# Kernel optimization log

Hardware: AMD Instinct MI355X
Metric: run time of the kernel (lower is better)

## Reference

```python
import jax, jax.numpy as jnp
import numpy as np

H = 128  # GRU hidden dim

def gru_sequence(x_emb, W_ih, W_hh, b_ih, b_hh):
    """Run a GRU over x_emb (S, B, E); return final-step output (B, H).
    Matches torch.nn.GRU gate math:
      r = sig(W_ir x + b_ir + W_hr h + b_hr)
      z = sig(W_iz x + b_iz + W_hz h + b_hz)
      n = tanh(W_in x + b_in + r * (W_hn h + b_hn))
      h' = (1 - z) * n + z * h
    """
    S, B, E = x_emb.shape
    # Precompute input projections for all timesteps: (S, B, 3H)
    gx_all = jnp.einsum('sbe,ge->sbg', x_emb, W_ih) + b_ih

    def step(h, gx):
        gh = h @ W_hh.T + b_hh               # (B, 3H)
        r = jax.nn.sigmoid(gx[:, :H] + gh[:, :H])
        z = jax.nn.sigmoid(gx[:, H:2*H] + gh[:, H:2*H])
        n = jnp.tanh(gx[:, 2*H:] + r * gh[:, 2*H:])
        h_new = (1.0 - z) * n + z * h
        return h_new, None

    h0 = jnp.zeros((B, H), dtype=x_emb.dtype)
    h_final, _ = jax.lax.scan(step, h0, gx_all)
    return h_final  # (B, H) == out at last timestep


def setup_inputs() -> dict:
    key = jax.random.key(0)
    ks = jax.random.split(key, 12)
    S, B, V, E = 512, 512, 50000, 50
    x1 = jax.random.randint(ks[0], (S, B), 0, V, dtype=jnp.int32)
    x2 = jax.random.randint(ks[1], (S, B), 0, V, dtype=jnp.int32)
    emb = jax.random.uniform(ks[2], (V, E), jnp.float32, -0.01, 0.01)
    s = 1.0 / np.sqrt(H)
    W_ih = jax.random.uniform(ks[3], (3*H, E), jnp.float32, -s, s)
    W_hh = jax.random.uniform(ks[4], (3*H, H), jnp.float32, -s, s)
    b_ih = jax.random.uniform(ks[5], (3*H,), jnp.float32, -s, s)
    b_hh = jax.random.uniform(ks[6], (3*H,), jnp.float32, -s, s)
    s1 = 1.0 / np.sqrt(2*H)
    W1 = jax.random.uniform(ks[7], (H, 2*H), jnp.float32, -s1, s1)
    b1 = jax.random.uniform(ks[8], (H,), jnp.float32, -s1, s1)
    s2 = 1.0 / np.sqrt(H)
    W2 = jax.random.uniform(ks[9], (1, H), jnp.float32, -s2, s2)
    b2 = jax.random.uniform(ks[10], (1,), jnp.float32, -s2, s2)
    return {"x1": x1, "x2": x2, "emb": emb, "W_ih": W_ih, "W_hh": W_hh,
            "b_ih": b_ih, "b_hh": b_hh, "W1": W1, "b1": b1, "W2": W2, "b2": b2}


def reference(x1, x2, emb, W_ih, W_hh, b_ih, b_hh, W1, b1, W2, b2):
    e1 = emb[x1]  # (S, B, E)
    e2 = emb[x2]
    h1 = gru_sequence(e1, W_ih, W_hh, b_ih, b_hh)  # (B, H)
    h2 = gru_sequence(e2, W_ih, W_hh, b_ih, b_hh)  # (B, H)
    fc_in = jnp.concatenate([h1, h2], axis=-1)     # (B, 2H)
    hid = jax.nn.relu(fc_in @ W1.T + b1)
    out = jax.nn.sigmoid(hid @ W2.T + b2)          # (B, 1)
    return out
```

## Files before the change

### kernel.cpp

```cpp
#include <hip/hip_runtime.h>
#include <hip/hip_bf16.h>
#include <stdint.h>

#define S_LEN 512
#define BATCH 512
#define HID   128
#define G3    384
#define EMB   50
#define VOC   50000

typedef __attribute__((ext_vector_type(8))) short short8;
typedef __attribute__((ext_vector_type(4))) float float4v;

__device__ inline unsigned short f2bf(float f) {
  union { float f; uint32_t u; } v; v.f = f;
  uint32_t u = v.u;
  u += 0x7fffu + ((u >> 16) & 1u);
  return (unsigned short)(u >> 16);
}
__device__ inline float bf2f(unsigned short h) {
  union { uint32_t u; float f; } v; v.u = ((uint32_t)h) << 16;
  return v.f;
}
__device__ inline uint32_t fbits(float f) {
  union { float f; uint32_t u; } v; v.f = f; return v.u;
}
__device__ inline float fast_sig(float x) {
  return __builtin_amdgcn_rcpf(1.f + __expf(-x));
}

__device__ inline short8 load8_bf_padded(const float* __restrict__ row, int k0) {
  float f[8];
  if (k0 + 7 < EMB) {
    float4v a = *(const float4v*)(row + k0);
    float4v b = *(const float4v*)(row + k0 + 4);
#pragma unroll
    for (int i = 0; i < 4; ++i) { f[i] = a[i]; f[i + 4] = b[i]; }
  } else {
#pragma unroll
    for (int i = 0; i < 8; ++i) f[i] = (k0 + i < EMB) ? row[k0 + i] : 0.f;
  }
  short8 s;
#pragma unroll
  for (int i = 0; i < 8; ++i) s[i] = (short)f2bf(f[i]);
  return s;
}

__global__ __launch_bounds__(256) void build_gxv(
    const float* __restrict__ emb, const float* __restrict__ W_ih,
    const float* __restrict__ b_ih, const float* __restrict__ b_hh,
    unsigned short* __restrict__ gxv) {
  __shared__ __align__(16) unsigned short cmat[64][392];
  const int w  = threadIdx.x >> 6;
  const int L  = threadIdx.x & 63;
  const int q  = L >> 4;
  const int ln = L & 15;
  const int vbase = blockIdx.x * 64 + w * 16;
  const int vloc  = w * 16;

  const int vr = min(vbase + ln, VOC - 1);
  const float* arow = emb + (size_t)vr * EMB;
  short8 afr0 = load8_bf_padded(arow, q * 8);
  short8 afr1 = load8_bf_padded(arow, 32 + q * 8);

  for (int nt = 0; nt < 24; ++nt) {
    const int gg = nt * 16 + ln;
    const float* brow = W_ih + (size_t)gg * EMB;
    short8 b0 = load8_bf_padded(brow, q * 8);
    short8 b1 = load8_bf_padded(brow, 32 + q * 8);
    const float bias = b_ih[gg] + (gg < 256 ? b_hh[gg] : 0.f);
    float4v acc = {bias, bias, bias, bias};
    acc = __builtin_amdgcn_mfma_f32_16x16x32_bf16(afr0, b0, acc, 0, 0, 0);
    acc = __builtin_amdgcn_mfma_f32_16x16x32_bf16(afr1, b1, acc, 0, 0, 0);
#pragma unroll
    for (int r = 0; r < 4; ++r)
      cmat[vloc + q * 4 + r][gg] = f2bf(acc[r]);
  }
  __syncthreads();

  for (int idx = threadIdx.x; idx < 3072; idx += 256) {
    const int row = idx / 48, c8 = idx - row * 48;
    const int vrow = blockIdx.x * 64 + row;
    if (vrow < VOC) {
      short8 v = *(const short8*)(&cmat[row][c8 * 8]);
      *(short8*)(gxv + (size_t)vrow * G3 + c8 * 8) = v;
    }
  }
}

__global__ __launch_bounds__(512) void gru_kernel(
    const int* __restrict__ x1, const int* __restrict__ x2,
    const unsigned short* __restrict__ gxv, const float* __restrict__ W_hh,
    const float* __restrict__ b_hh, float* __restrict__ fcin) {
  const int bid   = blockIdx.x;
  const int gru   = bid >> 7;
  const int chunk = bid & 127;
  const int* xs   = gru ? x2 : x1;

  const int tid = threadIdx.x;
  const int w  = tid >> 6;
  const int L  = tid & 63;
  const int q  = L >> 4;
  const int ln = L & 15;
  const int jb = w * 16;
  const int jl = L >> 2, n = L & 3;
  const int j  = jb + jl;
  const int ng = chunk * 4 + n;

  __shared__ __align__(16) unsigned short hbuf[2][512];
  __shared__ float scr[3][128][4];

  short8 afrag[3][4];
#pragma unroll
  for (int t = 0; t < 3; ++t) {
    const float* wr = W_hh + (size_t)(t * 128 + jb + ln) * HID;
#pragma unroll
    for (int kf = 0; kf < 4; ++kf) {
      const int k0 = kf * 32 + q * 8;
      float4v f0 = *(const float4v*)(wr + k0);
      float4v f1 = *(const float4v*)(wr + k0 + 4);
      short8 a;
#pragma unroll
      for (int i = 0; i < 4; ++i) a[i] = (short)f2bf(f0[i]);
#pragma unroll
      for (int i = 0; i < 4; ++i) a[i + 4] = (short)f2bf(f1[i]);
      afrag[t][kf] = a;
    }
  }

  const float bhn = b_hh[2 * 128 + j];

  for (int idx = tid; idx < 1024; idx += 512) ((unsigned short*)hbuf)[idx] = 0;

  float h = 0.f;

  const int tok0 = xs[ng];
  unsigned short gxr, gxz, gxnn;
  {
    const unsigned short* gp = gxv + (size_t)tok0 * G3;
    gxr = gp[j]; gxz = gp[128 + j]; gxnn = gp[256 + j];
  }
  int tok1 = xs[BATCH + ng];

  const int wofs = (((j >> 3) * 4 + n) << 3) + (j & 7);
  const int rofs = ((q * 4 + (ln & 3)) << 3);

  __syncthreads();

  for (int s = 0; s < S_LEN; ++s) {
    unsigned short pr, pz, pn;
    {
      const unsigned short* gp = gxv + (size_t)tok1 * G3;
      pr = gp[j]; pz = gp[128 + j]; pn = gp[256 + j];
    }
    const int s2 = (s + 2 < S_LEN) ? (s + 2) : 0;
    const int tok2 = xs[s2 * BATCH + ng];

    const unsigned short* rb = hbuf[s & 1];
    short8 bfrag[4];
#pragma unroll
    for (int kf = 0; kf < 4; ++kf)
      bfrag[kf] = *(const short8*)(rb + kf * 128 + rofs);

    float4v acc[3];
#pragma unroll
    for (int t = 0; t < 3; ++t) {
      float4v a0 = {0.f, 0.f, 0.f, 0.f};
      float4v a1 = {0.f, 0.f, 0.f, 0.f};
      a0 = __builtin_amdgcn_mfma_f32_16x16x32_bf16(afrag[t][0], bfrag[0], a0, 0, 0, 0);
      a1 = __builtin_amdgcn_mfma_f32_16x16x32_bf16(afrag[t][1], bfrag[1], a1, 0, 0, 0);
      a0 = __builtin_amdgcn_mfma_f32_16x16x32_bf16(afrag[t][2], bfrag[2], a0, 0, 0, 0);
      a1 = __builtin_amdgcn_mfma_f32_16x16x32_bf16(afrag[t][3], bfrag[3], a1, 0, 0, 0);
      acc[t] = a0 + a1;
    }

    if (ln < 4) {
#pragma unroll
      for (int t = 0; t < 3; ++t)
#pragma unroll
        for (int r = 0; r < 4; ++r)
          scr[t][jb + q * 4 + r][ln] = acc[t][r];
    }
    const float aR = scr[0][j][n];
    const float aZ = scr[1][j][n];
    const float aN = scr[2][j][n];

    const float gr  = bf2f(gxr) + aR;
    const float gz  = bf2f(gxz) + aZ;
    const float ghn = aN + bhn;
    const float rg  = fast_sig(gr);
    const float zg  = fast_sig(gz);
    const float pre = bf2f(gxnn) + rg * ghn;
    const float nn  = 2.f * fast_sig(2.f * pre) - 1.f;
    h = zg * (h - nn) + nn;

    hbuf[(s + 1) & 1][wofs] = (unsigned short)((fbits(h) + 0x8000u) >> 16);

    asm volatile("s_waitcnt lgkmcnt(0)\n\ts_barrier" ::: "memory");

    gxr = pr; gxz = pz; gxnn = pn;
    tok1 = tok2;
  }

  fcin[(size_t)ng * 256 + gru * 128 + j] = h;
}

__global__ __launch_bounds__(128) void head_kernel(
    const float* __restrict__ fcin, const float* __restrict__ W1,
    const float* __restrict__ b1, const float* __restrict__ W2,
    const float* __restrict__ b2, float* __restrict__ out) {
  __shared__ float fc[256];
  __shared__ float part[2];
  const int b = blockIdx.x, t = threadIdx.x;
  fc[t]       = fcin[(size_t)b * 256 + t];
  fc[t + 128] = fcin[(size_t)b * 256 + t + 128];
  __syncthreads();

  float acc = b1[t];
#pragma unroll 8
  for (int k = 0; k < 256; ++k) acc += W1[t * 256 + k] * fc[k];
  const float hid = fmaxf(acc, 0.f);

  float v = hid * W2[t];
#pragma unroll
  for (int o = 32; o > 0; o >>= 1) v += __shfl_xor(v, o, 64);
  if ((t & 63) == 0) part[t >> 6] = v;
  __syncthreads();
  if (t == 0) {
    const float s = part[0] + part[1] + b2[0];
    out[b] = fast_sig(s);
  }
}

extern "C" void kernel_launch(void* const* d_in, const int* in_sizes, int n_in,
                              void* d_out, int out_size, void* d_ws, size_t ws_size,
                              hipStream_t stream) {
  const int*   x1   = (const int*)d_in[0];
  const int*   x2   = (const int*)d_in[1];
  const float* emb  = (const float*)d_in[2];
  const float* W_ih = (const float*)d_in[3];
  const float* W_hh = (const float*)d_in[4];
  const float* b_ih = (const float*)d_in[5];
  const float* b_hh = (const float*)d_in[6];
  const float* W1   = (const float*)d_in[7];
  const float* b1   = (const float*)d_in[8];
  const float* W2   = (const float*)d_in[9];
  const float* b2   = (const float*)d_in[10];
  float* out = (float*)d_out;

  unsigned short* gxv = (unsigned short*)d_ws;
  float* fcin = (float*)((char*)d_ws + (size_t)VOC * G3 * 2);

  build_gxv<<<(VOC + 63) / 64, 256, 0, stream>>>(emb, W_ih, b_ih, b_hh, gxv);
  gru_kernel<<<256, 512, 0, stream>>>(x1, x2, gxv, W_hh, b_hh, fcin);
  head_kernel<<<512, 128, 0, stream>>>(fcin, W1, b1, W2, b2, out);
}
```

Measured before the change: 414.3 us.

## Fold exp2 scaling into weights, transpose gate scratch, and prefetch W_ih tiles

Pre-scales W_ih, W_hh and the biases by -log2(e) (or -2·log2(e) for the n gate), so the recurrent step can apply exp2 directly with no multiply before the sigmoid and tanh. The b_hn bias is loaded into the MFMA accumulator instead of being added afterwards. The gate scratch buffer is transposed and padded so each lane stores a float4 vector instead of four scalar stores. build_gxv also software-prefetches the next W_ih tile. The per-step dependency chain gets shorter, but bf16 rounding now applies to the scaled weights, which shifts numerics slightly.

```diff
diff --git a/kernel.cpp b/kernel.cpp
--- a/kernel.cpp
+++ b/kernel.cpp
@@ -9,6 +9,9 @@
 #define EMB   50
 #define VOC   50000
 
+#define NL2E  (-1.4426950408889634f)
+#define N2L2E (-2.8853900817779268f)
+
 typedef __attribute__((ext_vector_type(8))) short short8;
 typedef __attribute__((ext_vector_type(4))) float float4v;
 
@@ -29,7 +32,8 @@
   return __builtin_amdgcn_rcpf(1.f + __expf(-x));
 }
 
-__device__ inline short8 load8_bf_padded(const float* __restrict__ row, int k0) {
+__device__ inline short8 load8_bf_padded(const float* __restrict__ row, int k0,
+                                         float sc) {
   float f[8];
   if (k0 + 7 < EMB) {
     float4v a = *(const float4v*)(row + k0);
@@ -42,7 +46,7 @@
   }
   short8 s;
 #pragma unroll
-  for (int i = 0; i < 8; ++i) s[i] = (short)f2bf(f[i]);
+  for (int i = 0; i < 8; ++i) s[i] = (short)f2bf(f[i] * sc);
   return s;
 }
 
@@ -60,21 +64,32 @@
 
   const int vr = min(vbase + ln, VOC - 1);
   const float* arow = emb + (size_t)vr * EMB;
-  short8 afr0 = load8_bf_padded(arow, q * 8);
-  short8 afr1 = load8_bf_padded(arow, 32 + q * 8);
+  short8 afr0 = load8_bf_padded(arow, q * 8, 1.f);
+  short8 afr1 = load8_bf_padded(arow, 32 + q * 8, 1.f);
+
+  int gg = ln;
+  float sc = NL2E;
+  short8 b0 = load8_bf_padded(W_ih + (size_t)gg * EMB, q * 8, sc);
+  short8 b1 = load8_bf_padded(W_ih + (size_t)gg * EMB, 32 + q * 8, sc);
+  float bias = sc * (b_ih[gg] + b_hh[gg]);
 
   for (int nt = 0; nt < 24; ++nt) {
-    const int gg = nt * 16 + ln;
-    const float* brow = W_ih + (size_t)gg * EMB;
-    short8 b0 = load8_bf_padded(brow, q * 8);
-    short8 b1 = load8_bf_padded(brow, 32 + q * 8);
-    const float bias = b_ih[gg] + (gg < 256 ? b_hh[gg] : 0.f);
+    short8 nb0, nb1; float nbias;
+    if (nt < 23) {
+      const int g2 = (nt + 1) * 16 + ln;
+      const float s2 = (g2 < 256) ? NL2E : N2L2E;
+      const float* brow = W_ih + (size_t)g2 * EMB;
+      nb0 = load8_bf_padded(brow, q * 8, s2);
+      nb1 = load8_bf_padded(brow, 32 + q * 8, s2);
+      nbias = s2 * (b_ih[g2] + (g2 < 256 ? b_hh[g2] : 0.f));
+    }
     float4v acc = {bias, bias, bias, bias};
     acc = __builtin_amdgcn_mfma_f32_16x16x32_bf16(afr0, b0, acc, 0, 0, 0);
     acc = __builtin_amdgcn_mfma_f32_16x16x32_bf16(afr1, b1, acc, 0, 0, 0);
 #pragma unroll
     for (int r = 0; r < 4; ++r)
       cmat[vloc + q * 4 + r][gg] = f2bf(acc[r]);
+    gg += 16; b0 = nb0; b1 = nb1; bias = nbias;
   }
   __syncthreads();
 
@@ -108,11 +123,12 @@
   const int ng = chunk * 4 + n;
 
   __shared__ __align__(16) unsigned short hbuf[2][512];
-  __shared__ float scr[3][128][4];
+  __shared__ __align__(16) float scr[3][4][136];
 
   short8 afrag[3][4];
 #pragma unroll
   for (int t = 0; t < 3; ++t) {
+    const float sc = (t < 2) ? NL2E : N2L2E;
     const float* wr = W_hh + (size_t)(t * 128 + jb + ln) * HID;
 #pragma unroll
     for (int kf = 0; kf < 4; ++kf) {
@@ -121,14 +137,16 @@
       float4v f1 = *(const float4v*)(wr + k0 + 4);
       short8 a;
 #pragma unroll
-      for (int i = 0; i < 4; ++i) a[i] = (short)f2bf(f0[i]);
-#pragma unroll
-      for (int i = 0; i < 4; ++i) a[i + 4] = (short)f2bf(f1[i]);
+      for (int i = 0; i < 4; ++i) a[i] = (short)f2bf(f0[i] * sc);
+#pragma unroll
+      for (int i = 0; i < 4; ++i) a[i + 4] = (short)f2bf(f1[i] * sc);
       afrag[t][kf] = a;
     }
   }
 
-  const float bhn = b_hh[2 * 128 + j];
+  float4v bhn4;
+#pragma unroll
+  for (int r = 0; r < 4; ++r) bhn4[r] = N2L2E * b_hh[2 * 128 + jb + q * 4 + r];
 
   for (int idx = tid; idx < 1024; idx += 512) ((unsigned short*)hbuf)[idx] = 0;
 
@@ -165,7 +183,7 @@
     float4v acc[3];
 #pragma unroll
     for (int t = 0; t < 3; ++t) {
-      float4v a0 = {0.f, 0.f, 0.f, 0.f};
+      float4v a0 = (t == 2) ? bhn4 : (float4v){0.f, 0.f, 0.f, 0.f};
       float4v a1 = {0.f, 0.f, 0.f, 0.f};
       a0 = __builtin_amdgcn_mfma_f32_16x16x32_bf16(afrag[t][0], bfrag[0], a0, 0, 0, 0);
       a1 = __builtin_amdgcn_mfma_f32_16x16x32_bf16(afrag[t][1], bfrag[1], a1, 0, 0, 0);
@@ -177,21 +195,19 @@
     if (ln < 4) {
 #pragma unroll
       for (int t = 0; t < 3; ++t)
-#pragma unroll
-        for (int r = 0; r < 4; ++r)
-          scr[t][jb + q * 4 + r][ln] = acc[t][r];
-    }
-    const float aR = scr[0][j][n];
-    const float aZ = scr[1][j][n];
-    const float aN = scr[2][j][n];
-
-    const float gr  = bf2f(gxr) + aR;
-    const float gz  = bf2f(gxz) + aZ;
-    const float ghn = aN + bhn;
-    const float rg  = fast_sig(gr);
-    const float zg  = fast_sig(gz);
-    const float pre = bf2f(gxnn) + rg * ghn;
-    const float nn  = 2.f * fast_sig(2.f * pre) - 1.f;
+        *(float4v*)(&scr[t][ln][jb + q * 4]) = acc[t];
+    }
+    const float aR = scr[0][n][j];
+    const float aZ = scr[1][n][j];
+    const float aN = scr[2][n][j];
+
+    const float gr = bf2f(gxr) + aR;
+    const float gz = bf2f(gxz) + aZ;
+    const float rg = __builtin_amdgcn_rcpf(1.f + __builtin_amdgcn_exp2f(gr));
+    const float zg = __builtin_amdgcn_rcpf(1.f + __builtin_amdgcn_exp2f(gz));
+    const float pre = bf2f(gxnn) + rg * aN;
+    const float sg  = __builtin_amdgcn_rcpf(1.f + __builtin_amdgcn_exp2f(pre));
+    const float nn  = 2.f * sg - 1.f;
     h = zg * (h - nn) + nn;
 
     hbuf[(s + 1) & 1][wofs] = (unsigned short)((fbits(h) + 0x8000u) >> 16);
```

Measured after the change: 407.0 us. Within noise of the previous version (-1.8%).
